# Performance work log

Hardware: AMD Instinct MI355X
Metric: run time of the kernel (lower is better)

## Reference

```python
import jax, jax.numpy as jnp
import numpy as np

B, T, C = 2, 2048, 1024
E = 8            # num_experts
K = 2            # num_active (top-k)
H = 4 * C        # expert hidden dim


def setup_inputs() -> dict:
    key = jax.random.key(0)
    ks = jax.random.split(key, 8)
    s = 0.02
    return {
        "x": jax.random.normal(ks[0], (B, T, C), dtype=jnp.float32),
        "Wg": jax.random.normal(ks[1], (C, E), dtype=jnp.float32) * s,
        "bg": jnp.zeros((E,), dtype=jnp.float32),
        "W1": jax.random.normal(ks[2], (E, C, H), dtype=jnp.float32) * s,
        "b1": jnp.zeros((E, H), dtype=jnp.float32),
        "W2": jax.random.normal(ks[3], (E, H, C), dtype=jnp.float32) * s,
        "b2": jnp.zeros((E, C), dtype=jnp.float32),
    }


def reference(x, Wg, bg, W1, b1, W2, b2):
    Bs, Ts, Cs = x.shape
    x_flat = x.reshape(-1, Cs)                       # [N, C]
    gate_logits = x_flat @ Wg + bg                   # [N, E]
    gates = jax.nn.softmax(gate_logits, axis=-1)
    w, idx = jax.lax.top_k(gates, K)                 # [N, K]
    w = w / jnp.sum(w, axis=-1, keepdims=True)
    # combine[n, e] = sum_k w[n,k] * (idx[n,k] == e); zero for unrouted experts,
    # so weighting the dense per-expert output reproduces the masked scatter-add.
    combine = jnp.sum(jax.nn.one_hot(idx, E, dtype=x.dtype) * w[..., None], axis=1)  # [N, E]
    out = jnp.zeros_like(x_flat)
    for e in range(E):  # small fixed expert loop; GEMM-dominated
        h = jax.nn.gelu(x_flat @ W1[e] + b1[e], approximate=False)  # [N, H]
        y = h @ W2[e] + b2[e]                                       # [N, C]
        out = out + y * combine[:, e:e + 1]
    return out.reshape(Bs, Ts, Cs)
```

## Files before the change

### kernel.cpp

```cpp
#include <hip/hip_runtime.h>
#include <hip/hip_bf16.h>
#include <math.h>

#define NTOK  4096
#define CDIM  1024
#define HDIM  4096
#define NEXP  8
#define TOPK  2

using short8 = __attribute__((ext_vector_type(8))) short;
using f32x4  = __attribute__((ext_vector_type(4))) float;
using us4    = __attribute__((ext_vector_type(4))) unsigned short;

__device__ inline ushort f2bf(float f) {
    uint32_t u = __builtin_bit_cast(uint32_t, f);
    uint32_t r = (u + 0x7FFFu + ((u >> 16) & 1u)) >> 16;
    return (ushort)r;
}

__device__ __forceinline__ void gl_lds16(const void* g, void* l) {
    __builtin_amdgcn_global_load_lds(
        (const __attribute__((address_space(1))) void*)(void*)g,
        (__attribute__((address_space(3))) void*)l, 16, 0, 0);
}

__global__ __launch_bounds__(256)
void gate_kernel(const float* __restrict__ x, const float* __restrict__ Wg,
                 const float* __restrict__ bg, int* __restrict__ counts,
                 int* __restrict__ tlist, float* __restrict__ wslot,
                 ushort* __restrict__ xbf) {
    int wave = threadIdx.x >> 6, lane = threadIdx.x & 63;
    int t = blockIdx.x * 4 + wave;
    const float* xr = x + (size_t)t * CDIM;

    float acc[NEXP];
#pragma unroll
    for (int e = 0; e < NEXP; e++) acc[e] = 0.f;

#pragma unroll
    for (int i = 0; i < CDIM / 64; i++) {
        int c = lane + 64 * i;
        float xv = xr[c];
        xbf[(size_t)t * CDIM + c] = f2bf(xv);
        const float* wr = Wg + (size_t)c * NEXP;
#pragma unroll
        for (int e = 0; e < NEXP; e++) acc[e] += xv * wr[e];
    }
#pragma unroll
    for (int e = 0; e < NEXP; e++) {
        float v = acc[e];
        for (int off = 32; off > 0; off >>= 1) v += __shfl_xor(v, off);
        acc[e] = v + bg[e];
    }
    if (lane == 0) {
        int i1 = 0; float m1 = acc[0];
#pragma unroll
        for (int e = 1; e < NEXP; e++) if (acc[e] > m1) { m1 = acc[e]; i1 = e; }
        int i2 = -1; float m2 = -1e30f;
#pragma unroll
        for (int e = 0; e < NEXP; e++) if (e != i1 && acc[e] > m2) { m2 = acc[e]; i2 = e; }
        float w0 = 1.f / (1.f + expf(m2 - m1));
        float w1 = 1.f - w0;
        int p0 = atomicAdd(&counts[i1], 1);
        tlist[i1 * NTOK + p0] = t * 2;
        int p1 = atomicAdd(&counts[i2], 1);
        tlist[i2 * NTOK + p1] = t * 2 + 1;
        wslot[t * 2]     = w0;
        wslot[t * 2 + 1] = w1;
    }
}

__global__ __launch_bounds__(256)
void transpose_kernel(const float* __restrict__ in, ushort* __restrict__ out,
                      int R, int Ccols) {
    __shared__ float tile[64][68];
    int e = blockIdx.z;
    const float* src = in + (size_t)e * R * Ccols;
    ushort* dst = out + (size_t)e * Ccols * R;
    int c0 = blockIdx.x * 64, r0 = blockIdx.y * 64;
    int tid = threadIdx.x;
    int tx = tid & 15, ty = tid >> 4;
#pragma unroll
    for (int j = 0; j < 4; j++) {
        float4 v = *(const float4*)&src[(size_t)(r0 + ty + 16 * j) * Ccols + c0 + tx * 4];
        *(float4*)&tile[ty + 16 * j][tx * 4] = v;
    }
    __syncthreads();
#pragma unroll
    for (int j = 0; j < 4; j++) {
        int c = ty + 16 * j;
        us4 o;
#pragma unroll
        for (int i = 0; i < 4; i++) o[i] = f2bf(tile[tx * 4 + i][c]);
        *(us4*)&dst[(size_t)(c0 + c) * R + r0 + tx * 4] = o;
    }
}

template<int GELU, int OUTBF16>
__global__ __launch_bounds__(256)
void moe_gemm(const ushort* __restrict__ A, const ushort* __restrict__ Bt,
              const float* __restrict__ bias, const int* __restrict__ tlist,
              const int* __restrict__ counts, void* __restrict__ Out,
              int K, int N, int ashift) {
    int e = blockIdx.z;
    int cnt = counts[e];
    int m0 = blockIdx.y * 128;
    if (m0 >= cnt) return;
    int n0 = blockIdx.x * 128;

    __shared__ ushort As[128 * 32];
    __shared__ ushort Bs[128 * 32];
    __shared__ int rowv[128];

    int tid = threadIdx.x;
    if (tid < 128) {
        int r = m0 + tid;
        rowv[tid] = tlist[e * NTOK + (r < cnt ? r : cnt - 1)];
    }
    __syncthreads();

    const ushort* Be = Bt + (size_t)e * N * K;

    f32x4 acc[4][4] = {};

    int lane = tid & 63, w = tid >> 6;
    int wm = (w >> 1) * 64, wn = (w & 1) * 64;
    int quad = lane >> 4, l16 = lane & 15;

    int srow = tid >> 2;
    int scol = (tid & 3) * 8;

    for (int kt = 0; kt < K; kt += 32) {
#pragma unroll
        for (int s = 0; s < 2; s++) {
            int row = srow + s * 64;
            const ushort* ap = A + (size_t)(rowv[row] >> ashift) * K + kt + scol;
            gl_lds16(ap, &As[(w * 16 + s * 64) * 32]);
            const ushort* bp = Be + (size_t)(n0 + row) * K + kt + scol;
            gl_lds16(bp, &Bs[(w * 16 + s * 64) * 32]);
        }
        __syncthreads();

        short8 a[4], b[4];
#pragma unroll
        for (int mt = 0; mt < 4; mt++)
            a[mt] = *(short8*)&As[(wm + mt * 16 + l16) * 32 + quad * 8];
#pragma unroll
        for (int nt = 0; nt < 4; nt++)
            b[nt] = *(short8*)&Bs[(wn + nt * 16 + l16) * 32 + quad * 8];
#pragma unroll
        for (int mt = 0; mt < 4; mt++)
#pragma unroll
            for (int nt = 0; nt < 4; nt++)
                acc[mt][nt] = __builtin_amdgcn_mfma_f32_16x16x32_bf16(
                    a[mt], b[nt], acc[mt][nt], 0, 0, 0);
        __syncthreads();
    }

    float* outF = (float*)Out;
    ushort* outH = (ushort*)Out;
    const float* be = bias + (size_t)e * N;
#pragma unroll
    for (int mt = 0; mt < 4; mt++) {
#pragma unroll
        for (int r = 0; r < 4; r++) {
            int lrow = wm + mt * 16 + quad * 4 + r;
            if (m0 + lrow < cnt) {
                int v = rowv[lrow];
                size_t base = (size_t)v * N;
#pragma unroll
                for (int nt = 0; nt < 4; nt++) {
                    int col = n0 + wn + nt * 16 + l16;
                    float val = acc[mt][nt][r] + be[col];
                    if (GELU) val = 0.5f * val * (1.0f + erff(val * 0.70710678118654752f));
                    if (OUTBF16) outH[base + col] = f2bf(val);
                    else         outF[base + col] = val;
                }
            }
        }
    }
}

__global__ __launch_bounds__(256)
void combine_kernel(const float* __restrict__ y, const float* __restrict__ wslot,
                    float* __restrict__ out) {
    int idx = blockIdx.x * 256 + threadIdx.x;
    int c4 = idx & (CDIM / 4 - 1);
    int t = idx >> 8;
    float w0 = wslot[2 * t], w1 = wslot[2 * t + 1];
    const float4* y0 = (const float4*)(y + (size_t)(2 * t) * CDIM);
    const float4* y1 = (const float4*)(y + (size_t)(2 * t + 1) * CDIM);
    float4 a = y0[c4], b = y1[c4], o;
    o.x = w0 * a.x + w1 * b.x;
    o.y = w0 * a.y + w1 * b.y;
    o.z = w0 * a.z + w1 * b.z;
    o.w = w0 * a.w + w1 * b.w;
    ((float4*)(out + (size_t)t * CDIM))[c4] = o;
}

extern "C" void kernel_launch(void* const* d_in, const int* in_sizes, int n_in,
                              void* d_out, int out_size, void* d_ws, size_t ws_size,
                              hipStream_t stream) {
    const float* x  = (const float*)d_in[0];
    const float* Wg = (const float*)d_in[1];
    const float* bg = (const float*)d_in[2];
    const float* W1 = (const float*)d_in[3];
    const float* b1 = (const float*)d_in[4];
    const float* W2 = (const float*)d_in[5];
    const float* b2 = (const float*)d_in[6];
    float* out = (float*)d_out;
    char* ws = (char*)d_ws;

    size_t off = 0;
    int*    counts = (int*)(ws + off);    off += 256;
    int*    tlist  = (int*)(ws + off);    off += (size_t)NEXP * NTOK * 4;
    float*  wslot  = (float*)(ws + off);  off += (size_t)NTOK * TOPK * 4;
    ushort* xbf    = (ushort*)(ws + off); off += (size_t)NTOK * CDIM * 2;
    ushort* WT     = (ushort*)(ws + off); off += (size_t)NEXP * CDIM * HDIM * 2;
    ushort* h      = (ushort*)(ws + off); off += (size_t)NTOK * TOPK * HDIM * 2;
    float*  y      = (float*)(ws + off);  off += (size_t)NTOK * TOPK * CDIM * 4;

    hipMemsetAsync(counts, 0, NEXP * sizeof(int), stream);

    gate_kernel<<<NTOK / 4, 256, 0, stream>>>(x, Wg, bg, counts, tlist, wslot, xbf);

    transpose_kernel<<<dim3(HDIM / 64, CDIM / 64, NEXP), 256, 0, stream>>>(
        W1, WT, CDIM, HDIM);

    moe_gemm<1, 1><<<dim3(HDIM / 128, NTOK / 128, NEXP), 256, 0, stream>>>(
        xbf, WT, b1, tlist, counts, (void*)h, CDIM, HDIM, 1);

    transpose_kernel<<<dim3(CDIM / 64, HDIM / 64, NEXP), 256, 0, stream>>>(
        W2, WT, HDIM, CDIM);

    moe_gemm<0, 0><<<dim3(CDIM / 128, NTOK / 128, NEXP), 256, 0, stream>>>(
        h, WT, b2, tlist, counts, (void*)y, HDIM, CDIM, 0);

    combine_kernel<<<(NTOK * CDIM / 4) / 256, 256, 0, stream>>>(y, wslot, out);
}
```

Measured before the change: 701.7 us.

## Pack routed tokens contiguously per expert, widen K tile, fuse combine into GEMM2

```diff
diff --git a/kernel.cpp b/kernel.cpp
--- a/kernel.cpp
+++ b/kernel.cpp
@@ -6,11 +6,12 @@
 #define CDIM  1024
 #define HDIM  4096
 #define NEXP  8
-#define TOPK  2
+#define MAXROWS (NTOK * 2 + NEXP * 128)
 
 using short8 = __attribute__((ext_vector_type(8))) short;
 using f32x4  = __attribute__((ext_vector_type(4))) float;
 using us4    = __attribute__((ext_vector_type(4))) unsigned short;
+using us8    = __attribute__((ext_vector_type(8))) unsigned short;
 
 __device__ inline ushort f2bf(float f) {
     uint32_t u = __builtin_bit_cast(uint32_t, f);
@@ -27,8 +28,7 @@
 __global__ __launch_bounds__(256)
 void gate_kernel(const float* __restrict__ x, const float* __restrict__ Wg,
                  const float* __restrict__ bg, int* __restrict__ counts,
-                 int* __restrict__ tlist, float* __restrict__ wslot,
-                 ushort* __restrict__ xbf) {
+                 int4* __restrict__ tchoice, float2* __restrict__ tw) {
     int wave = threadIdx.x >> 6, lane = threadIdx.x & 63;
     int t = blockIdx.x * 4 + wave;
     const float* xr = x + (size_t)t * CDIM;
@@ -41,7 +41,6 @@
     for (int i = 0; i < CDIM / 64; i++) {
         int c = lane + 64 * i;
         float xv = xr[c];
-        xbf[(size_t)t * CDIM + c] = f2bf(xv);
         const float* wr = Wg + (size_t)c * NEXP;
 #pragma unroll
         for (int e = 0; e < NEXP; e++) acc[e] += xv * wr[e];
@@ -62,103 +61,134 @@
         float w0 = 1.f / (1.f + expf(m2 - m1));
         float w1 = 1.f - w0;
         int p0 = atomicAdd(&counts[i1], 1);
-        tlist[i1 * NTOK + p0] = t * 2;
         int p1 = atomicAdd(&counts[i2], 1);
-        tlist[i2 * NTOK + p1] = t * 2 + 1;
-        wslot[t * 2]     = w0;
-        wslot[t * 2 + 1] = w1;
+        tchoice[t] = make_int4(i1, p0, i2, p1);
+        tw[t] = make_float2(w0, w1);
+    }
+}
+
+__global__ void scan_kernel(const int* __restrict__ counts, int* __restrict__ bases) {
+    if (threadIdx.x == 0) {
+        int b = 0;
+        for (int e = 0; e < NEXP; e++) {
+            bases[e] = b;
+            b += ((counts[e] + 127) >> 7) << 7;
+        }
+    }
+}
+
+__global__ __launch_bounds__(256)
+void pack_kernel(const float* __restrict__ x, const int4* __restrict__ tchoice,
+                 const float2* __restrict__ tw, const int* __restrict__ bases,
+                 ushort* __restrict__ xpack, float* __restrict__ wpack,
+                 int* __restrict__ tokpack) {
+    int t = blockIdx.x, tid = threadIdx.x;
+    int4 ch = tchoice[t];
+    float2 wv = tw[t];
+    int d1 = bases[ch.x] + ch.y;
+    int d2 = bases[ch.z] + ch.w;
+    float4 v = ((const float4*)(x + (size_t)t * CDIM))[tid];
+    us4 o;
+    o[0] = f2bf(v.x); o[1] = f2bf(v.y); o[2] = f2bf(v.z); o[3] = f2bf(v.w);
+    *(us4*)&xpack[(size_t)d1 * CDIM + tid * 4] = o;
+    *(us4*)&xpack[(size_t)d2 * CDIM + tid * 4] = o;
+    if (tid == 0) {
+        wpack[d1] = wv.x; tokpack[d1] = t;
+        wpack[d2] = wv.y; tokpack[d2] = t;
     }
 }
 
 __global__ __launch_bounds__(256)
 void transpose_kernel(const float* __restrict__ in, ushort* __restrict__ out,
-                      int R, int Ccols) {
-    __shared__ float tile[64][68];
+                      int R, int Cc) {
+    __shared__ float tile[64 * 65];
     int e = blockIdx.z;
-    const float* src = in + (size_t)e * R * Ccols;
-    ushort* dst = out + (size_t)e * Ccols * R;
+    const float* src = in + (size_t)e * R * Cc;
+    ushort* dst = out + (size_t)e * Cc * R;
     int c0 = blockIdx.x * 64, r0 = blockIdx.y * 64;
-    int tid = threadIdx.x;
-    int tx = tid & 15, ty = tid >> 4;
+    int tid = threadIdx.x, tx = tid & 15, ty = tid >> 4;
 #pragma unroll
     for (int j = 0; j < 4; j++) {
-        float4 v = *(const float4*)&src[(size_t)(r0 + ty + 16 * j) * Ccols + c0 + tx * 4];
-        *(float4*)&tile[ty + 16 * j][tx * 4] = v;
+        float4 v = *(const float4*)&src[(size_t)(r0 + ty + 16 * j) * Cc + c0 + tx * 4];
+        int base = (ty + 16 * j) * 65 + tx * 4;
+        tile[base + 0] = v.x; tile[base + 1] = v.y;
+        tile[base + 2] = v.z; tile[base + 3] = v.w;
     }
     __syncthreads();
-#pragma unroll
-    for (int j = 0; j < 4; j++) {
-        int c = ty + 16 * j;
-        us4 o;
-#pragma unroll
-        for (int i = 0; i < 4; i++) o[i] = f2bf(tile[tx * 4 + i][c]);
-        *(us4*)&dst[(size_t)(c0 + c) * R + r0 + tx * 4] = o;
-    }
-}
-
-template<int GELU, int OUTBF16>
+    int rb = tid & 7, ccb = tid >> 3;
+#pragma unroll
+    for (int p = 0; p < 2; p++) {
+        int cc = ccb + 32 * p;
+        us8 o;
+#pragma unroll
+        for (int i = 0; i < 8; i++) o[i] = f2bf(tile[(rb * 8 + i) * 65 + cc]);
+        *(us8*)&dst[(size_t)(c0 + cc) * R + r0 + rb * 8] = o;
+    }
+}
+
+template<int GELU, int ATOMIC>
 __global__ __launch_bounds__(256)
 void moe_gemm(const ushort* __restrict__ A, const ushort* __restrict__ Bt,
-              const float* __restrict__ bias, const int* __restrict__ tlist,
-              const int* __restrict__ counts, void* __restrict__ Out,
-              int K, int N, int ashift) {
-    int e = blockIdx.z;
-    int cnt = counts[e];
-    int m0 = blockIdx.y * 128;
+              const float* __restrict__ bias, const int* __restrict__ counts,
+              const int* __restrict__ bases, ushort* __restrict__ outH,
+              float* __restrict__ outA, const float* __restrict__ wpack,
+              const int* __restrict__ tokpack, int K, int N) {
+    int bz = blockIdx.z;
+    int e  = ATOMIC ? (bz >> 1) : bz;
+    int kh = ATOMIC ? (bz & 1) : 0;
+    int kspan = ATOMIC ? (K >> 1) : K;
+    int k0 = kh * kspan;
+
+    int cnt = counts[e], base = bases[e];
+    int m0 = blockIdx.x * 128;
     if (m0 >= cnt) return;
-    int n0 = blockIdx.x * 128;
-
-    __shared__ ushort As[128 * 32];
-    __shared__ ushort Bs[128 * 32];
-    __shared__ int rowv[128];
-
-    int tid = threadIdx.x;
-    if (tid < 128) {
-        int r = m0 + tid;
-        rowv[tid] = tlist[e * NTOK + (r < cnt ? r : cnt - 1)];
-    }
-    __syncthreads();
-
+    int n0 = blockIdx.y * 128;
+
+    const ushort* Ae = A + (size_t)base * K;
     const ushort* Be = Bt + (size_t)e * N * K;
 
-    f32x4 acc[4][4] = {};
-
-    int lane = tid & 63, w = tid >> 6;
+    __shared__ ushort As[128 * 64];
+    __shared__ ushort Bs[128 * 64];
+
+    int tid = threadIdx.x, lane = tid & 63, w = tid >> 6;
     int wm = (w >> 1) * 64, wn = (w & 1) * 64;
     int quad = lane >> 4, l16 = lane & 15;
-
-    int srow = tid >> 2;
-    int scol = (tid & 3) * 8;
-
-    for (int kt = 0; kt < K; kt += 32) {
-#pragma unroll
-        for (int s = 0; s < 2; s++) {
-            int row = srow + s * 64;
-            const ushort* ap = A + (size_t)(rowv[row] >> ashift) * K + kt + scol;
-            gl_lds16(ap, &As[(w * 16 + s * 64) * 32]);
-            const ushort* bp = Be + (size_t)(n0 + row) * K + kt + scol;
-            gl_lds16(bp, &Bs[(w * 16 + s * 64) * 32]);
+    int rm = l16 & 7;
+    int xo0 = ((quad ^ rm) << 3);
+
+    int srow = tid >> 3;
+    int cg   = (tid & 7) ^ (srow & 7);
+
+    f32x4 acc[4][4] = {};
+
+    for (int kt = k0; kt < k0 + kspan; kt += 64) {
+#pragma unroll
+        for (int s = 0; s < 4; s++) {
+            int row = s * 32 + srow;
+            gl_lds16(Ae + (size_t)(m0 + row) * K + kt + cg * 8, &As[(s * 32 + w * 8) * 64]);
+            gl_lds16(Be + (size_t)(n0 + row) * K + kt + cg * 8, &Bs[(s * 32 + w * 8) * 64]);
         }
         __syncthreads();
-
-        short8 a[4], b[4];
-#pragma unroll
-        for (int mt = 0; mt < 4; mt++)
-            a[mt] = *(short8*)&As[(wm + mt * 16 + l16) * 32 + quad * 8];
-#pragma unroll
-        for (int nt = 0; nt < 4; nt++)
-            b[nt] = *(short8*)&Bs[(wn + nt * 16 + l16) * 32 + quad * 8];
-#pragma unroll
-        for (int mt = 0; mt < 4; mt++)
+#pragma unroll
+        for (int ks = 0; ks < 2; ks++) {
+            int xo = xo0 ^ (ks << 5);
+            short8 a[4], b[4];
+#pragma unroll
+            for (int mt = 0; mt < 4; mt++)
+                a[mt] = *(short8*)&As[(wm + mt * 16 + l16) * 64 + xo];
 #pragma unroll
             for (int nt = 0; nt < 4; nt++)
-                acc[mt][nt] = __builtin_amdgcn_mfma_f32_16x16x32_bf16(
-                    a[mt], b[nt], acc[mt][nt], 0, 0, 0);
+                b[nt] = *(short8*)&Bs[(wn + nt * 16 + l16) * 64 + xo];
+#pragma unroll
+            for (int mt = 0; mt < 4; mt++)
+#pragma unroll
+                for (int nt = 0; nt < 4; nt++)
+                    acc[mt][nt] = __builtin_amdgcn_mfma_f32_16x16x32_bf16(
+                        a[mt], b[nt], acc[mt][nt], 0, 0, 0);
+        }
         __syncthreads();
     }
 
-    float* outF = (float*)Out;
-    ushort* outH = (ushort*)Out;
     const float* be = bias + (size_t)e * N;
 #pragma unroll
     for (int mt = 0; mt < 4; mt++) {
@@ -166,36 +196,30 @@
         for (int r = 0; r < 4; r++) {
             int lrow = wm + mt * 16 + quad * 4 + r;
             if (m0 + lrow < cnt) {
-                int v = rowv[lrow];
-                size_t base = (size_t)v * N;
-#pragma unroll
-                for (int nt = 0; nt < 4; nt++) {
-                    int col = n0 + wn + nt * 16 + l16;
-                    float val = acc[mt][nt][r] + be[col];
-                    if (GELU) val = 0.5f * val * (1.0f + erff(val * 0.70710678118654752f));
-                    if (OUTBF16) outH[base + col] = f2bf(val);
-                    else         outF[base + col] = val;
+                int prow = base + m0 + lrow;
+                if (GELU) {
+                    size_t ob = (size_t)prow * N;
+#pragma unroll
+                    for (int nt = 0; nt < 4; nt++) {
+                        int col = n0 + wn + nt * 16 + l16;
+                        float val = acc[mt][nt][r] + be[col];
+                        val = 0.5f * val * (1.0f + erff(val * 0.70710678118654752f));
+                        outH[ob + col] = f2bf(val);
+                    }
+                } else {
+                    float wv = wpack[prow];
+                    size_t ob = (size_t)tokpack[prow] * CDIM;
+#pragma unroll
+                    for (int nt = 0; nt < 4; nt++) {
+                        int col = n0 + wn + nt * 16 + l16;
+                        float val = acc[mt][nt][r];
+                        if (kh == 0) val += be[col];
+                        atomicAdd(&outA[ob + col], val * wv);
+                    }
                 }
             }
         }
     }
-}
-
-__global__ __launch_bounds__(256)
-void combine_kernel(const float* __restrict__ y, const float* __restrict__ wslot,
-                    float* __restrict__ out) {
-    int idx = blockIdx.x * 256 + threadIdx.x;
-    int c4 = idx & (CDIM / 4 - 1);
-    int t = idx >> 8;
-    float w0 = wslot[2 * t], w1 = wslot[2 * t + 1];
-    const float4* y0 = (const float4*)(y + (size_t)(2 * t) * CDIM);
-    const float4* y1 = (const float4*)(y + (size_t)(2 * t + 1) * CDIM);
-    float4 a = y0[c4], b = y1[c4], o;
-    o.x = w0 * a.x + w1 * b.x;
-    o.y = w0 * a.y + w1 * b.y;
-    o.z = w0 * a.z + w1 * b.z;
-    o.w = w0 * a.w + w1 * b.w;
-    ((float4*)(out + (size_t)t * CDIM))[c4] = o;
 }
 
 extern "C" void kernel_launch(void* const* d_in, const int* in_sizes, int n_in,
@@ -212,29 +236,34 @@
     char* ws = (char*)d_ws;
 
     size_t off = 0;
-    int*    counts = (int*)(ws + off);    off += 256;
-    int*    tlist  = (int*)(ws + off);    off += (size_t)NEXP * NTOK * 4;
-    float*  wslot  = (float*)(ws + off);  off += (size_t)NTOK * TOPK * 4;
-    ushort* xbf    = (ushort*)(ws + off); off += (size_t)NTOK * CDIM * 2;
-    ushort* WT     = (ushort*)(ws + off); off += (size_t)NEXP * CDIM * HDIM * 2;
-    ushort* h      = (ushort*)(ws + off); off += (size_t)NTOK * TOPK * HDIM * 2;
-    float*  y      = (float*)(ws + off);  off += (size_t)NTOK * TOPK * CDIM * 4;
-
-    hipMemsetAsync(counts, 0, NEXP * sizeof(int), stream);
-
-    gate_kernel<<<NTOK / 4, 256, 0, stream>>>(x, Wg, bg, counts, tlist, wslot, xbf);
+    int*    counts  = (int*)(ws + off);    off += 256;
+    int*    bases   = (int*)(ws + off);    off += 256;
+    int4*   tchoice = (int4*)(ws + off);   off += (size_t)NTOK * 16;
+    float2* tw      = (float2*)(ws + off); off += (size_t)NTOK * 8;
+    float*  wpack   = (float*)(ws + off);  off += (size_t)MAXROWS * 4;
+    int*    tokpack = (int*)(ws + off);    off += (size_t)MAXROWS * 4;
+    off = (off + 255) & ~(size_t)255;
+    ushort* xpack   = (ushort*)(ws + off); off += (size_t)MAXROWS * CDIM * 2;
+    ushort* WT      = (ushort*)(ws + off); off += (size_t)NEXP * CDIM * HDIM * 2;
+    ushort* h       = (ushort*)(ws + off); off += (size_t)MAXROWS * HDIM * 2;
+
+    hipMemsetAsync(counts, 0, 2 * 256, stream);
+    hipMemsetAsync(xpack, 0, (size_t)MAXROWS * CDIM * 2, stream);
+    hipMemsetAsync(out, 0, (size_t)NTOK * CDIM * 4, stream);
+
+    gate_kernel<<<NTOK / 4, 256, 0, stream>>>(x, Wg, bg, counts, tchoice, tw);
+    scan_kernel<<<1, 64, 0, stream>>>(counts, bases);
+    pack_kernel<<<NTOK, 256, 0, stream>>>(x, tchoice, tw, bases, xpack, wpack, tokpack);
 
     transpose_kernel<<<dim3(HDIM / 64, CDIM / 64, NEXP), 256, 0, stream>>>(
         W1, WT, CDIM, HDIM);
 
-    moe_gemm<1, 1><<<dim3(HDIM / 128, NTOK / 128, NEXP), 256, 0, stream>>>(
-        xbf, WT, b1, tlist, counts, (void*)h, CDIM, HDIM, 1);
+    moe_gemm<1, 0><<<dim3(32, HDIM / 128, NEXP), 256, 0, stream>>>(
+        xpack, WT, b1, counts, bases, h, nullptr, nullptr, nullptr, CDIM, HDIM);
 
     transpose_kernel<<<dim3(CDIM / 64, HDIM / 64, NEXP), 256, 0, stream>>>(
         W2, WT, HDIM, CDIM);
 
-    moe_gemm<0, 0><<<dim3(CDIM / 128, NTOK / 128, NEXP), 256, 0, stream>>>(
-        h, WT, b2, tlist, counts, (void*)y, HDIM, CDIM, 0);
-
-    combine_kernel<<<(NTOK * CDIM / 4) / 256, 256, 0, stream>>>(y, wslot, out);
-}
+    moe_gemm<0, 1><<<dim3(32, CDIM / 128, NEXP * 2), 256, 0, stream>>>(
+        h, WT, b2, counts, bases, nullptr, out, wpack, tokpack, HDIM, CDIM);
+}
```

New measurement: 1.371 ms. 95.4% more time.
